# Kernel optimization log

Measured on AMD Instinct MI355X. Metric: run time of the kernel, lower is better.

## Reference

```python
import jax, jax.numpy as jnp
import numpy as np

D = 64      # in_feats
OUT = 64    # out_feats
MEM = 4     # mem_size
NREL = 8    # num_rels
N = 20000   # num nodes
E = 50000   # num edges
FF = 16     # dim_feedforward (hardcoded in module)
NH = 4      # nhead (hardcoded)
EPS = 1e-5  # LayerNorm eps (torch default)


def _ln(x, w, b):
    m = x.mean(-1, keepdims=True)
    v = ((x - m) ** 2).mean(-1, keepdims=True)
    return (x - m) * jax.lax.rsqrt(v + EPS) * w + b


def _enc(x, Wqkv, bqkv, Wo, bo, W1, b1, W2, b2, ln1w, ln1b, ln2w, ln2b):
    # torch TransformerEncoderLayer, batch_first, post-norm, eval mode, no padding mask (all-zero mask)
    B, S, d = x.shape
    dh = d // NH
    qkv = x @ Wqkv.T + bqkv
    q, k, v = jnp.split(qkv, 3, axis=-1)
    q = q.reshape(B, S, NH, dh)
    k = k.reshape(B, S, NH, dh)
    v = v.reshape(B, S, NH, dh)
    att = jax.nn.softmax(jnp.einsum('bqhd,bkhd->bhqk', q, k) / jnp.sqrt(jnp.float32(dh)), axis=-1)
    o = jnp.einsum('bhqk,bkhd->bqhd', att, v).reshape(B, S, d) @ Wo.T + bo
    x = _ln(x + o, ln1w, ln1b)
    ff = jax.nn.relu(x @ W1.T + b1) @ W2.T + b2
    return _ln(x + ff, ln2w, ln2b)


def setup_inputs() -> dict:
    key = jax.random.key(0)
    ks = jax.random.split(key, 16)
    s = 0.05
    inp = {
        'feat': jax.random.normal(ks[0], (N, D), jnp.float32),
        'src_idx': jax.random.randint(ks[1], (E,), 0, N),
        'dst_idx': jax.random.randint(ks[2], (E,), 0, N),
        'etype': jax.random.randint(ks[3], (E,), 0, NREL),
        'Wqkv': jax.random.normal(ks[4], (3 * D, D), jnp.float32) * s,
        'bqkv': jnp.zeros((3 * D,), jnp.float32),
        'Wo': jax.random.normal(ks[5], (D, D), jnp.float32) * s,
        'bo': jnp.zeros((D,), jnp.float32),
        'W1': jax.random.normal(ks[6], (FF, D), jnp.float32) * s,
        'b1': jnp.zeros((FF,), jnp.float32),
        'W2': jax.random.normal(ks[7], (D, FF), jnp.float32) * s,
        'b2': jnp.zeros((D,), jnp.float32),
        'ln1w': jnp.ones((D,), jnp.float32),
        'ln1b': jnp.zeros((D,), jnp.float32),
        'ln2w': jnp.ones((D,), jnp.float32),
        'ln2b': jnp.zeros((D,), jnp.float32),
        'Wc': jax.random.normal(ks[8], (MEM, D), jnp.float32) * s,
        'bc': jnp.zeros((MEM,), jnp.float32),
        'CLS': jax.random.normal(ks[9], (MEM, D), jnp.float32),
        'SEP': jax.random.normal(ks[10], (D,), jnp.float32),
        'Wm': jax.random.normal(ks[11], (OUT * D, D), jnp.float32) * s,
        'h_bias': jnp.zeros((OUT,), jnp.float32),
    }
    return inp


def reference(feat, src_idx, dst_idx, etype, Wqkv, bqkv, Wo, bo, W1, b1, W2, b2,
              ln1w, ln1b, ln2w, ln2b, Wc, bc, CLS, SEP, Wm, h_bias):
    enc_args = (Wqkv, bqkv, Wo, bo, W1, b1, W2, b2, ln1w, ln1b, ln2w, ln2b)

    def cls_pass(s_, d_):
        # run the shared encoder MEM times with a different CLS token; the math
        # is identical for every relation type, so no per-etype partition needed
        B = s_.shape[0]
        outs = []
        mem = jnp.zeros((B, D), s_.dtype)
        for i in range(MEM):
            cls = jnp.broadcast_to(CLS[i], (B, D))[:, None, :]
            sep = jnp.broadcast_to(SEP, (B, D))[:, None, :]
            seq = jnp.concatenate([cls, s_[:, None, :], sep, d_[:, None, :]], axis=1)  # [B,4,D]
            t = _enc(seq, *enc_args)[:, 0, :]
            outs.append(t)
            mem = mem + t
        return mem, jnp.stack(outs)  # [B,D], [MEM,B,D]

    src = feat[src_idx]  # [E,D]
    dst = feat[dst_idx]
    mem_emb, tmps = cls_pass(src, dst)
    cat_all = tmps @ Wc.T + bc               # [MEM,E,MEM]
    w = (mem_emb @ Wm.T).reshape(E, OUT, D)  # per-edge hypernetwork weight
    msg = jnp.einsum('eoi,ei->eo', w, src)   # [E,OUT]

    # dgl fn.mean aggregation over destination nodes (0 for isolated nodes)
    cnt = jax.ops.segment_sum(jnp.ones((E,), msg.dtype), dst_idx, num_segments=N)
    agg = jax.ops.segment_sum(msg, dst_idx, num_segments=N)
    node_rep = jnp.where(cnt[:, None] > 0, agg / jnp.maximum(cnt, 1.0)[:, None], 0.0)
    node_rep = node_rep + h_bias

    # self loop (same hypernetwork path over every node)
    mem_s, _ = cls_pass(feat, feat)
    hs = (mem_s @ Wm.T).reshape(N, OUT, D)
    node_rep = node_rep + jnp.einsum('noi,ni->no', hs, feat)

    # reconstruct torch concat order of category/label: outer loop etype, inner loop mem idx
    et = etype.astype(jnp.int32)
    counts = jax.ops.segment_sum(jnp.ones((E,), jnp.int32), etype, num_segments=NREL)
    start = jnp.concatenate([jnp.zeros((1,), jnp.int32), jnp.cumsum(counts)[:-1].astype(jnp.int32)])
    order = jnp.argsort(etype, stable=True)
    rank = jnp.zeros((E,), jnp.int32).at[order].set(jnp.arange(E, dtype=jnp.int32) - start[et[order]])
    base = start[et] * MEM + rank                                            # [E]
    pos = base[None, :] + jnp.arange(MEM, dtype=jnp.int32)[:, None] * counts[et][None, :]  # [MEM,E]
    category = jnp.zeros((MEM * E, MEM), cat_all.dtype).at[pos.reshape(-1)].set(cat_all.reshape(-1, MEM))
    label = jnp.zeros((MEM * E,), jnp.int32).at[pos.reshape(-1)].set(
        jnp.repeat(jnp.arange(MEM, dtype=jnp.int32), E))
    return node_rep, label, category
```

## Files before the change

### kernel.cpp

```cpp
#include <hip/hip_runtime.h>
#include <hip/hip_bf16.h>

typedef float f32x4_t __attribute__((ext_vector_type(4)));
typedef short bf16x8_t __attribute__((ext_vector_type(8)));

#define MFMA(a, b, c) __builtin_amdgcn_mfma_f32_16x16x32_bf16(a, b, c, 0, 0, 0)

#define C_Q0   0
#define C_S00  256
#define C_S02  272
#define C_VCLS 288
#define C_VSEP 544

__device__ __forceinline__ short f2bf(float x) {
    return (short)__builtin_bit_cast(unsigned short, __float2bfloat16(x));
}
__device__ __forceinline__ float bf2f(short s) {
    return __builtin_bit_cast(float, ((unsigned)(unsigned short)s) << 16);
}
__device__ __forceinline__ float head_sum16(float v) {
#pragma unroll
    for (int off = 1; off < 16; off <<= 1) v += __shfl_xor(v, off, 64);
    return v;
}

__global__ void k_pack(const float* __restrict__ Wo, const float* __restrict__ Wqkv,
                       const float* __restrict__ W1, const float* __restrict__ W2,
                       const float* __restrict__ Wm, const float* __restrict__ Wc,
                       short* __restrict__ Bpack, short* __restrict__ WoP,
                       short* __restrict__ WkvP, short* __restrict__ W1P,
                       short* __restrict__ W2P, short* __restrict__ WcP)
{
    int tid = blockIdx.x * 256 + threadIdx.x;
    short tmp[8];
    if (tid < 32768) {
        int u = tid, lane = u & 63, nt = (u >> 6) & 3, kstep = u >> 8;
        int o = nt * 16 + (lane & 15);
        int kb = kstep * 32 + (lane >> 4) * 8;
#pragma unroll
        for (int t = 0; t < 8; t++) { int k = kb + t; tmp[t] = f2bf(Wm[(o * 64 + (k >> 6)) * 64 + (k & 63)]); }
        *(bf16x8_t*)&Bpack[(size_t)u * 8] = *(bf16x8_t*)tmp;
    } else if (tid < 33280) {
        int u = tid - 32768, lane = u & 63, nt = (u >> 6) & 3, kstep = u >> 8;
        int o = nt * 16 + (lane & 15), kb = kstep * 32 + (lane >> 4) * 8;
#pragma unroll
        for (int t = 0; t < 8; t++) tmp[t] = f2bf(Wo[o * 64 + kb + t]);
        *(bf16x8_t*)&WoP[(size_t)u * 8] = *(bf16x8_t*)tmp;
    } else if (tid < 34304) {
        int u = tid - 33280, lane = u & 63, nt = (u >> 6) & 7, kstep = u >> 9;
        int col = nt * 16 + (lane & 15), kb = kstep * 32 + (lane >> 4) * 8;
        int row = 64 + col;
#pragma unroll
        for (int t = 0; t < 8; t++) tmp[t] = f2bf(Wqkv[row * 64 + kb + t]);
        *(bf16x8_t*)&WkvP[(size_t)u * 8] = *(bf16x8_t*)tmp;
    } else if (tid < 34432) {
        int u = tid - 34304, lane = u & 63, kstep = u >> 6;
        int f = lane & 15, kb = kstep * 32 + (lane >> 4) * 8;
#pragma unroll
        for (int t = 0; t < 8; t++) tmp[t] = f2bf(W1[f * 64 + kb + t]);
        *(bf16x8_t*)&W1P[(size_t)u * 8] = *(bf16x8_t*)tmp;
    } else if (tid < 34688) {
        int u = tid - 34432, lane = u & 63, nt = u >> 6;
        int o = nt * 16 + (lane & 15), kb = (lane >> 4) * 8;
#pragma unroll
        for (int t = 0; t < 8; t++) { int k = kb + t; tmp[t] = (k < 16) ? f2bf(W2[o * 16 + k]) : (short)0; }
        *(bf16x8_t*)&W2P[(size_t)u * 8] = *(bf16x8_t*)tmp;
    } else if (tid < 34816) {
        int u = tid - 34688, lane = u & 63, kstep = u >> 6;
        int m = lane & 15, kb = kstep * 32 + (lane >> 4) * 8;
#pragma unroll
        for (int t = 0; t < 8; t++) tmp[t] = (m < 4) ? f2bf(Wc[m * 64 + kb + t]) : (short)0;
        *(bf16x8_t*)&WcP[(size_t)u * 8] = *(bf16x8_t*)tmp;
    }
}

__global__ void k_small(const float* __restrict__ Wqkv, const float* __restrict__ bqkv,
                        const float* __restrict__ CLS, const float* __restrict__ SEP,
                        float* __restrict__ consts)
{
    int lane = threadIdx.x;
    float ksep = bqkv[64 + lane], vsep = bqkv[128 + lane];
    for (int c = 0; c < 64; c++) {
        float sc = SEP[c];
        ksep += Wqkv[(64 + lane) * 64 + c] * sc;
        vsep += Wqkv[(128 + lane) * 64 + c] * sc;
    }
    consts[C_VSEP + lane] = vsep;
    for (int i = 0; i < 4; i++) {
        float q0 = bqkv[lane], kcls = bqkv[64 + lane], vcls = bqkv[128 + lane];
        for (int c = 0; c < 64; c++) {
            float cc = CLS[i * 64 + c];
            q0   += Wqkv[lane * 64 + c] * cc;
            kcls += Wqkv[(64 + lane) * 64 + c] * cc;
            vcls += Wqkv[(128 + lane) * 64 + c] * cc;
        }
        consts[C_Q0 + i * 64 + lane] = q0;
        consts[C_VCLS + i * 64 + lane] = vcls;
        float p00 = head_sum16(q0 * kcls) * 0.25f;
        float p02 = head_sum16(q0 * ksep) * 0.25f;
        if ((lane & 15) == 0) {
            consts[C_S00 + i * 4 + (lane >> 4)] = p00;
            consts[C_S02 + i * 4 + (lane >> 4)] = p02;
        }
    }
}

__global__ __launch_bounds__(256) void k_kv(const float* __restrict__ feat,
        const short* __restrict__ WkvP, const float* __restrict__ bqkv,
        float* __restrict__ knode, float* __restrict__ vnode, int N)
{
    __shared__ __align__(16) short sA[64 * 72];
    int tid = threadIdx.x, lane = tid & 63, w = tid >> 6;
    int l15 = lane & 15, lh = lane >> 4;
    int base = blockIdx.x * 64;
#pragma unroll
    for (int rr = 0; rr < 16; rr++) {
        int row = w * 16 + rr;
        int n = base + row; n = n < N ? n : N - 1;
        sA[row * 72 + lane] = f2bf(feat[(size_t)n * 64 + lane]);
    }
    __syncthreads();
    const bf16x8_t* bp = (const bf16x8_t*)WkvP;
    bf16x8_t bk0 = bp[(0 * 8 + w) * 64 + lane];
    bf16x8_t bk1 = bp[(1 * 8 + w) * 64 + lane];
    bf16x8_t bv0 = bp[(0 * 8 + 4 + w) * 64 + lane];
    bf16x8_t bv1 = bp[(1 * 8 + 4 + w) * 64 + lane];
    int kof = lh * 8;
    int col = w * 16 + l15;
    float biask = bqkv[64 + col], biasv = bqkv[128 + col];
#pragma unroll
    for (int rt = 0; rt < 4; rt++) {
        bf16x8_t a0 = *(const bf16x8_t*)&sA[(rt * 16 + l15) * 72 + kof];
        bf16x8_t a1 = *(const bf16x8_t*)&sA[(rt * 16 + l15) * 72 + 32 + kof];
        f32x4_t ak = {0.f, 0.f, 0.f, 0.f}, av = ak;
        ak = MFMA(a0, bk0, ak); ak = MFMA(a1, bk1, ak);
        av = MFMA(a0, bv0, av); av = MFMA(a1, bv1, av);
#pragma unroll
        for (int r = 0; r < 4; r++) {
            int n = base + rt * 16 + lh * 4 + r;
            if (n < N) {
                knode[(size_t)n * 64 + col] = ak[r] + biask;
                vnode[(size_t)n * 64 + col] = av[r] + biasv;
            }
        }
    }
}

struct EncW {
    const float* consts; const float* CLS; const float* bo;
    const float* b1; const float* b2;
    const float* ln1w; const float* ln1b; const float* ln2w; const float* ln2b;
    const short* WoP; const short* W1P; const short* W2P; const short* WcP;
    const float* bc;
};

__global__ __launch_bounds__(256) void k_enc(const int* __restrict__ src_idx,
        const int* __restrict__ dst_idx,
        const float* __restrict__ knode, const float* __restrict__ vnode, EncW W,
        float* __restrict__ mem_out, float* __restrict__ cat_out, int E, int M)
{
    __shared__ __align__(16) short sA[64 * 72];
    __shared__ __align__(16) short sF[64 * 40];
    int tid = threadIdx.x, lane = tid & 63, w = tid >> 6;
    int l15 = lane & 15, lh = lane >> 4;
    int base = blockIdx.x * 16;

#pragma unroll
    for (int z = 0; z < 4; z++) {
        int zz = z * 64 + lane;
        sF[(w * 16 + (zz >> 4)) * 40 + 16 + (zz & 15)] = 0;
    }

    float q0r[4], vclsr[4], s00r[4], s02r[4];
#pragma unroll
    for (int i = 0; i < 4; i++) {
        q0r[i]   = W.consts[C_Q0 + i * 64 + lane];
        vclsr[i] = W.consts[C_VCLS + i * 64 + lane];
        s00r[i]  = W.consts[C_S00 + i * 4 + lh];
        s02r[i]  = W.consts[C_S02 + i * 4 + lh];
    }
    float vsep = W.consts[C_VSEP + lane];

#pragma unroll
    for (int el = 0; el < 4; el++) {
        int eloc = w * 4 + el;
        int ge = base + eloc; int gc = ge < M ? ge : M - 1;
        int s, d;
        if (gc < E) { s = src_idx[gc]; d = dst_idx[gc]; }
        else        { s = gc - E; d = s; }
        float ks = knode[(size_t)s * 64 + lane], vs_ = vnode[(size_t)s * 64 + lane];
        float kd = knode[(size_t)d * 64 + lane], vd  = vnode[(size_t)d * 64 + lane];
#pragma unroll
        for (int i = 0; i < 4; i++) {
            float s01 = head_sum16(q0r[i] * ks) * 0.25f;
            float s03 = head_sum16(q0r[i] * kd) * 0.25f;
            float s00 = s00r[i], s02 = s02r[i];
            float mx = fmaxf(fmaxf(s00, s01), fmaxf(s02, s03));
            float e0 = __expf(s00 - mx), e1 = __expf(s01 - mx);
            float e2 = __expf(s02 - mx), e3 = __expf(s03 - mx);
            float inv = 1.0f / (e0 + e1 + e2 + e3);
            float att = (e0 * vclsr[i] + e1 * vs_ + e2 * vsep + e3 * vd) * inv;
            sA[(eloc * 4 + i) * 72 + lane] = f2bf(att);
        }
    }

    int arow = (w * 16 + l15) * 72;
    int kof = lh * 8;

    const bf16x8_t* bpo = (const bf16x8_t*)W.WoP;
    f32x4_t ac0 = {0.f,0.f,0.f,0.f}, ac1 = ac0, ac2 = ac0, ac3 = ac0;
#pragma unroll
    for (int kstep = 0; kstep < 2; kstep++) {
        bf16x8_t a = *(const bf16x8_t*)&sA[arow + kstep * 32 + kof];
        ac0 = MFMA(a, bpo[(kstep * 4 + 0) * 64 + lane], ac0);
        ac1 = MFMA(a, bpo[(kstep * 4 + 1) * 64 + lane], ac1);
        ac2 = MFMA(a, bpo[(kstep * 4 + 2) * 64 + lane], ac2);
        ac3 = MFMA(a, bpo[(kstep * 4 + 3) * 64 + lane], ac3);
    }

    float x[4][4], y[4][4];
#pragma unroll
    for (int r = 0; r < 4; r++) { x[0][r] = ac0[r]; x[1][r] = ac1[r]; x[2][r] = ac2[r]; x[3][r] = ac3[r]; }
    float lw1[4], lb1[4];
#pragma unroll
    for (int nt = 0; nt < 4; nt++) {
        float b = W.bo[nt * 16 + l15];
        lw1[nt] = W.ln1w[nt * 16 + l15]; lb1[nt] = W.ln1b[nt * 16 + l15];
#pragma unroll
        for (int r = 0; r < 4; r++) x[nt][r] += b + W.CLS[r * 64 + nt * 16 + l15];
    }
#pragma unroll
    for (int r = 0; r < 4; r++) {
        float sm = head_sum16(x[0][r] + x[1][r] + x[2][r] + x[3][r]);
        float mu = sm * 0.015625f;
        float vv = 0.f;
#pragma unroll
        for (int nt = 0; nt < 4; nt++) { float dd = x[nt][r] - mu; vv = fmaf(dd, dd, vv); }
        vv = head_sum16(vv);
        float rs = rsqrtf(vv * 0.015625f + 1e-5f);
#pragma unroll
        for (int nt = 0; nt < 4; nt++) y[nt][r] = (x[nt][r] - mu) * rs * lw1[nt] + lb1[nt];
    }
#pragma unroll
    for (int nt = 0; nt < 4; nt++)
#pragma unroll
        for (int r = 0; r < 4; r++)
            sA[(w * 16 + lh * 4 + r) * 72 + nt * 16 + l15] = f2bf(y[nt][r]);

    const bf16x8_t* bp1 = (const bf16x8_t*)W.W1P;
    f32x4_t fa = {0.f,0.f,0.f,0.f};
#pragma unroll
    for (int kstep = 0; kstep < 2; kstep++) {
        bf16x8_t a = *(const bf16x8_t*)&sA[arow + kstep * 32 + kof];
        fa = MFMA(a, bp1[kstep * 64 + lane], fa);
    }
    float b1v = W.b1[l15];
#pragma unroll
    for (int r = 0; r < 4; r++)
        sF[(w * 16 + lh * 4 + r) * 40 + l15] = f2bf(fmaxf(fa[r] + b1v, 0.f));

    const bf16x8_t* bp2 = (const bf16x8_t*)W.W2P;
    bf16x8_t af = *(const bf16x8_t*)&sF[(w * 16 + l15) * 40 + kof];
    f32x4_t z0 = {0.f,0.f,0.f,0.f}, z1 = z0, z2 = z0, z3 = z0;
    z0 = MFMA(af, bp2[0 * 64 + lane], z0);
    z1 = MFMA(af, bp2[1 * 64 + lane], z1);
    z2 = MFMA(af, bp2[2 * 64 + lane], z2);
    z3 = MFMA(af, bp2[3 * 64 + lane], z3);

    float t[4][4];
#pragma unroll
    for (int r = 0; r < 4; r++) { x[0][r] = z0[r]; x[1][r] = z1[r]; x[2][r] = z2[r]; x[3][r] = z3[r]; }
    float lw2[4], lb2[4];
#pragma unroll
    for (int nt = 0; nt < 4; nt++) {
        float b = W.b2[nt * 16 + l15];
        lw2[nt] = W.ln2w[nt * 16 + l15]; lb2[nt] = W.ln2b[nt * 16 + l15];
#pragma unroll
        for (int r = 0; r < 4; r++) x[nt][r] += b + y[nt][r];
    }
#pragma unroll
    for (int r = 0; r < 4; r++) {
        float sm = head_sum16(x[0][r] + x[1][r] + x[2][r] + x[3][r]);
        float mu = sm * 0.015625f;
        float vv = 0.f;
#pragma unroll
        for (int nt = 0; nt < 4; nt++) { float dd = x[nt][r] - mu; vv = fmaf(dd, dd, vv); }
        vv = head_sum16(vv);
        float rs = rsqrtf(vv * 0.015625f + 1e-5f);
#pragma unroll
        for (int nt = 0; nt < 4; nt++) t[nt][r] = (x[nt][r] - mu) * rs * lw2[nt] + lb2[nt];
    }

    int eloc = w * 4 + lh, ge = base + eloc;

    if (base < E) {
#pragma unroll
        for (int nt = 0; nt < 4; nt++)
#pragma unroll
            for (int r = 0; r < 4; r++)
                sA[(w * 16 + lh * 4 + r) * 72 + nt * 16 + l15] = f2bf(t[nt][r]);
        const bf16x8_t* bpc = (const bf16x8_t*)W.WcP;
        f32x4_t ca = {0.f,0.f,0.f,0.f};
#pragma unroll
        for (int kstep = 0; kstep < 2; kstep++) {
            bf16x8_t a = *(const bf16x8_t*)&sA[arow + kstep * 32 + kof];
            ca = MFMA(a, bpc[kstep * 64 + lane], ca);
        }
        if (l15 < 4 && ge < E) {
            float bcv = W.bc[l15];
#pragma unroll
            for (int r = 0; r < 4; r++)
                cat_out[((size_t)r * E + ge) * 4 + l15] = ca[r] + bcv;
        }
    }

    if (ge < M) {
#pragma unroll
        for (int nt = 0; nt < 4; nt++)
            mem_out[(size_t)ge * 64 + nt * 16 + l15] = t[nt][0] + t[nt][1] + t[nt][2] + t[nt][3];
    }
}

__global__ __launch_bounds__(256, 3) void k_hyper(
        const float* __restrict__ feat, const int* __restrict__ src_idx,
        const int* __restrict__ dst_idx, const float* __restrict__ memall,
        const short* __restrict__ Bpack,
        float* __restrict__ agg, float* __restrict__ selfm, int E, int M)
{
    __shared__ short xsT[64 * 132];
    __shared__ __align__(16) short sB[2][8192];
    int tid = threadIdx.x, lane = tid & 63, w = tid >> 6;
    int l15 = lane & 15, lh = lane >> 4, koff = lh * 8;
    int base = blockIdx.x * 128;

    const bf16x8_t* bp = (const bf16x8_t*)Bpack;

    auto stage = [&](int c, int buf) {
#pragma unroll
        for (int jj = 0; jj < 4; ++jj) {
            int j = w * 4 + jj;
            int il_ic = j >> 3, q = j & 7;
            const short* src = (const short*)(bp + (size_t)(c * 2 + il_ic) * 512
                                              + (q >> 2) * 256 + (q & 3) * 64 + lane);
            short* dst = &sB[buf][j * 512];
            __builtin_amdgcn_global_load_lds(
                (const __attribute__((address_space(1))) void*)src,
                (__attribute__((address_space(3))) void*)dst, 16, 0, 0);
        }
    };

    stage(0, 0);

    for (int rr = 0; rr < 32; ++rr) {
        int row = w * 32 + rr, gr = base + row;
        float xv = 0.f;
        if (gr < M) {
            int xi = gr < E ? src_idx[gr] : gr - E;
            xv = feat[(size_t)xi * 64 + lane];
        }
        xsT[lane * 132 + row] = f2bf(xv);
    }

    bf16x8_t am[2][2];
#pragma unroll
    for (int tt = 0; tt < 2; ++tt) {
        int gr = base + w * 32 + tt * 16 + l15;
        const float* mp = memall + (size_t)(gr < M ? gr : 0) * 64 + koff;
#pragma unroll
        for (int kk = 0; kk < 2; ++kk)
#pragma unroll
            for (int t = 0; t < 8; ++t)
                am[tt][kk][t] = f2bf(mp[kk * 32 + t]);
    }

    f32x4_t out[2][4];
#pragma unroll
    for (int tt = 0; tt < 2; ++tt)
#pragma unroll
        for (int nt = 0; nt < 4; ++nt) out[tt][nt] = (f32x4_t){0.f, 0.f, 0.f, 0.f};
    const f32x4_t ZERO = {0.f, 0.f, 0.f, 0.f};

    int xrow0 = w * 32 + lh * 4;

    int cur = 0;
    for (int c = 0; c < 32; ++c) {
        if (c + 1 < 32) {
            stage(c + 1, cur ^ 1);
            asm volatile("s_waitcnt vmcnt(4)" ::: "memory");
        } else {
            asm volatile("s_waitcnt vmcnt(0)" ::: "memory");
        }
        __builtin_amdgcn_s_barrier();
#pragma unroll
        for (int ic = 0; ic < 2; ++ic) {
            int i = c * 2 + ic;
            unsigned long long xw0 = *(const unsigned long long*)&xsT[i * 132 + xrow0];
            unsigned long long xw1 = *(const unsigned long long*)&xsT[i * 132 + xrow0 + 16];
            float x0[4], x1[4];
            {
                unsigned lo0 = (unsigned)xw0, hi0 = (unsigned)(xw0 >> 32);
                unsigned lo1 = (unsigned)xw1, hi1 = (unsigned)(xw1 >> 32);
                x0[0] = __builtin_bit_cast(float, lo0 << 16);
                x0[1] = __builtin_bit_cast(float, lo0 & 0xffff0000u);
                x0[2] = __builtin_bit_cast(float, hi0 << 16);
                x0[3] = __builtin_bit_cast(float, hi0 & 0xffff0000u);
                x1[0] = __builtin_bit_cast(float, lo1 << 16);
                x1[1] = __builtin_bit_cast(float, lo1 & 0xffff0000u);
                x1[2] = __builtin_bit_cast(float, hi1 << 16);
                x1[3] = __builtin_bit_cast(float, hi1 & 0xffff0000u);
            }
            const bf16x8_t* bfr = (const bf16x8_t*)&sB[cur][ic * 4096];
            f32x4_t P0[4], P1[4];
            __builtin_amdgcn_s_setprio(1);
#pragma unroll
            for (int nt = 0; nt < 4; ++nt) {
                bf16x8_t B0 = bfr[nt * 64 + lane];
                bf16x8_t B1 = bfr[(4 + nt) * 64 + lane];
                P0[nt] = MFMA(am[0][0], B0, ZERO);
                P1[nt] = MFMA(am[1][0], B0, ZERO);
                P0[nt] = MFMA(am[0][1], B1, P0[nt]);
                P1[nt] = MFMA(am[1][1], B1, P1[nt]);
            }
            __builtin_amdgcn_s_setprio(0);
#pragma unroll
            for (int nt = 0; nt < 4; ++nt)
#pragma unroll
                for (int r = 0; r < 4; ++r) {
                    out[0][nt][r] = fmaf(x0[r], P0[nt][r], out[0][nt][r]);
                    out[1][nt][r] = fmaf(x1[r], P1[nt][r], out[1][nt][r]);
                }
        }
        __builtin_amdgcn_s_barrier();
        cur ^= 1;
    }

#pragma unroll
    for (int tt = 0; tt < 2; ++tt) {
        int orow = w * 32 + tt * 16 + lh * 4;
        int di[4];
#pragma unroll
        for (int r = 0; r < 4; ++r) {
            int grow = base + orow + r;
            di[r] = (grow < E) ? dst_idx[grow] : 0;
        }
#pragma unroll
        for (int nt = 0; nt < 4; ++nt) {
            int o = nt * 16 + l15;
#pragma unroll
            for (int r = 0; r < 4; ++r) {
                int grow = base + orow + r;
                if (grow < M) {
                    float v = out[tt][nt][r];
                    if (grow < E) atomicAdd(&agg[(size_t)di[r] * 64 + o], v);
                    else selfm[(size_t)(grow - E) * 64 + o] = v;
                }
            }
        }
    }
}

__global__ void k_fin(const float* __restrict__ agg, const int* __restrict__ cnt,
                      const float* __restrict__ selfm, const float* __restrict__ h_bias,
                      float* __restrict__ outp, int N)
{
    int t = blockIdx.x * 256 + threadIdx.x;
    if (t < N * 64) {
        int n = t >> 6, o = t & 63;
        int c = cnt[n];
        float av = (c > 0) ? agg[t] / (float)c : 0.f;
        outp[t] = av + h_bias[o] + selfm[t];
    }
}

__global__ void k_hist(const int* __restrict__ etype, const int* __restrict__ dst,
                       int* __restrict__ hist, int* __restrict__ cnt, int E)
{
    __shared__ int h[8];
    int tid = threadIdx.x;
    if (tid < 8) h[tid] = 0;
    __syncthreads();
    int e = blockIdx.x * 256 + tid;
    if (e < E) {
        atomicAdd(&h[etype[e]], 1);
        atomicAdd(&cnt[dst[e]], 1);
    }
    __syncthreads();
    if (tid < 8) hist[blockIdx.x * 8 + tid] = h[tid];
}

__global__ void k_scan(const int* __restrict__ hist, int* __restrict__ chunkoff,
                       int* __restrict__ startg, int* __restrict__ countsg, int nch)
{
    int lane = threadIdx.x;
    int g = lane & 7, seg = lane >> 3;
    int per = (nch + 7) / 8;
    int c0 = seg * per, c1 = c0 + per; if (c1 > nch) c1 = nch;
    int sum = 0;
    for (int c = c0; c < c1; c++) sum += hist[c * 8 + g];
    int pre = 0, tot = 0;
#pragma unroll
    for (int s2 = 0; s2 < 8; s2++) {
        int v = __shfl(sum, s2 * 8 + g, 64);
        tot += v;
        if (s2 < seg) pre += v;
    }
    int run = pre;
    for (int c = c0; c < c1; c++) { chunkoff[c * 8 + g] = run; run += hist[c * 8 + g]; }
    if (seg == 0) {
        countsg[g] = tot;
        int sg = 0;
#pragma unroll
        for (int g2 = 0; g2 < 8; g2++) { int v = __shfl(tot, g2, 64); if (g2 < g) sg += v; }
        startg[g] = sg;
    }
}

__global__ __launch_bounds__(256) void k_scatter(const int* __restrict__ etype,
        const float* __restrict__ cat_all,
        const int* __restrict__ chunkoff, const int* __restrict__ startg,
        const int* __restrict__ countsg,
        float* __restrict__ out_label, float* __restrict__ out_cat, int E)
{
    __shared__ int wc[4][8];
    int tid = threadIdx.x, lane = tid & 63, w = tid >> 6;
    int chunk = blockIdx.x;
    int e = chunk * 256 + w * 64 + lane;
    int et = (e < E) ? etype[e] : -1;
    unsigned long long mk[8];
#pragma unroll
    for (int g = 0; g < 8; g++) mk[g] = __ballot(et == g);
    if (lane < 8) wc[w][lane] = (int)__popcll(mk[lane]);
    __syncthreads();
    if (et >= 0) {
        unsigned long long lt = (1ull << lane) - 1ull;
        int myr = chunkoff[chunk * 8 + et] + (int)__popcll(mk[et] & lt);
#pragma unroll
        for (int w2 = 0; w2 < 4; w2++) if (w2 < w) myr += wc[w2][et];
        int sg = startg[et], cg = countsg[et];
        size_t pbase = (size_t)sg * 4 + myr;
#pragma unroll
        for (int i = 0; i < 4; i++) {
            size_t pos = pbase + (size_t)i * cg;
            out_label[pos] = (float)i;
            const float* ca = &cat_all[((size_t)i * E + e) * 4];
            float4 cv = {ca[0], ca[1], ca[2], ca[3]};
            *(float4*)&out_cat[pos * 4] = cv;
        }
    }
}

extern "C" void kernel_launch(void* const* d_in, const int* in_sizes, int n_in,
                              void* d_out, int out_size, void* d_ws, size_t ws_size,
                              hipStream_t stream)
{
    const float* feat    = (const float*)d_in[0];
    const int*   src_idx = (const int*)d_in[1];
    const int*   dst_idx = (const int*)d_in[2];
    const int*   etype   = (const int*)d_in[3];
    const float* Wqkv    = (const float*)d_in[4];
    const float* bqkv    = (const float*)d_in[5];
    const float* Wo      = (const float*)d_in[6];
    const float* bo      = (const float*)d_in[7];
    const float* W1      = (const float*)d_in[8];
    const float* b1      = (const float*)d_in[9];
    const float* W2      = (const float*)d_in[10];
    const float* b2      = (const float*)d_in[11];
    const float* ln1w    = (const float*)d_in[12];
    const float* ln1b    = (const float*)d_in[13];
    const float* ln2w    = (const float*)d_in[14];
    const float* ln2b    = (const float*)d_in[15];
    const float* Wc      = (const float*)d_in[16];
    const float* bc      = (const float*)d_in[17];
    const float* CLS     = (const float*)d_in[18];
    const float* SEP     = (const float*)d_in[19];
    const float* Wm      = (const float*)d_in[20];
    const float* h_bias  = (const float*)d_in[21];

    const int N = in_sizes[0] / 64;
    const int E = in_sizes[1];
    const int M = E + N;
    const int NCH = (E + 255) / 256;

    float* ws = (float*)d_ws;
    size_t off = 0;
    auto alloc = [&](size_t n) { float* p = ws + off; off += (n + 63) & ~(size_t)63; return p; };
    float* knode   = alloc((size_t)N * 64);
    float* vnode   = alloc((size_t)N * 64);
    float* mem_all = alloc((size_t)M * 64);
    float* cat_all = alloc((size_t)E * 16);
    float* agg     = alloc((size_t)N * 64 + N);
    int*   cnt     = (int*)(agg + (size_t)N * 64);
    float* selfm   = alloc((size_t)N * 64);
    float* consts  = alloc(1024);
    short* Bpack   = (short*)alloc(131072);
    short* WoP     = (short*)alloc(2048);
    short* WkvP    = (short*)alloc(4096);
    short* W1P     = (short*)alloc(512);
    short* W2P     = (short*)alloc(1024);
    short* WcP     = (short*)alloc(512);
    int*   hist    = (int*)alloc(NCH * 8);
    int*   chunkoff= (int*)alloc(NCH * 8);
    int*   startg  = (int*)alloc(8);
    int*   countsg = (int*)alloc(8);

    float* out_node  = (float*)d_out;
    float* out_label = out_node + (size_t)N * 64;
    float* out_cat   = out_label + (size_t)4 * E;

    hipMemsetAsync(agg, 0, ((size_t)N * 64 + N) * sizeof(float), stream);

    k_pack<<<136, 256, 0, stream>>>(Wo, Wqkv, W1, W2, Wm, Wc, Bpack, WoP, WkvP, W1P, W2P, WcP);
    k_small<<<1, 64, 0, stream>>>(Wqkv, bqkv, CLS, SEP, consts);
    k_hist<<<NCH, 256, 0, stream>>>(etype, dst_idx, hist, cnt, E);
    k_scan<<<1, 64, 0, stream>>>(hist, chunkoff, startg, countsg, NCH);

    k_kv<<<(N + 63) / 64, 256, 0, stream>>>(feat, WkvP, bqkv, knode, vnode, N);

    EncW W{consts, CLS, bo, b1, b2, ln1w, ln1b, ln2w, ln2b, WoP, W1P, W2P, WcP, bc};

    k_enc<<<(M + 15) / 16, 256, 0, stream>>>(src_idx, dst_idx, knode, vnode, W,
                                             mem_all, cat_all, E, M);

    k_hyper<<<(M + 127) / 128, 256, 0, stream>>>(feat, src_idx, dst_idx, mem_all, Bpack,
                                                 agg, selfm, E, M);

    k_fin<<<(N * 64 + 255) / 256, 256, 0, stream>>>(agg, cnt, selfm, h_bias, out_node, N);

    k_scatter<<<NCH, 256, 0, stream>>>(etype, cat_all, chunkoff, startg, countsg,
                                       out_label, out_cat, E);
}
```

Baseline: 165.3 us.

## Merge prep kernels and widen hypernetwork tile to 256 rows with 512 threads

Three small setup kernels (weight packing, constant computation, histogram) are fused into one launch by dispatching on block index, which removes launch gaps. The hypernetwork kernel now processes 256 rows per block with 8 waves, so each staged Bpack chunk is reused across twice as many rows and global weight traffic is halved. The staging granularity drops to one i-slice per iteration, using a single barrier per step with a full vmcnt wait. Shorter prefetch chunks and more barriers per row could expose load latency, and the larger block may reduce occupancy.

```diff
diff --git a/kernel.cpp b/kernel.cpp
--- a/kernel.cpp
+++ b/kernel.cpp
@@ -24,84 +24,102 @@
     return v;
 }
 
-__global__ void k_pack(const float* __restrict__ Wo, const float* __restrict__ Wqkv,
+__global__ void k_prep(const float* __restrict__ Wo, const float* __restrict__ Wqkv,
                        const float* __restrict__ W1, const float* __restrict__ W2,
                        const float* __restrict__ Wm, const float* __restrict__ Wc,
+                       const float* __restrict__ bqkv,
+                       const float* __restrict__ CLS, const float* __restrict__ SEP,
+                       const int* __restrict__ etype, const int* __restrict__ dst,
                        short* __restrict__ Bpack, short* __restrict__ WoP,
                        short* __restrict__ WkvP, short* __restrict__ W1P,
-                       short* __restrict__ W2P, short* __restrict__ WcP)
-{
-    int tid = blockIdx.x * 256 + threadIdx.x;
-    short tmp[8];
-    if (tid < 32768) {
-        int u = tid, lane = u & 63, nt = (u >> 6) & 3, kstep = u >> 8;
-        int o = nt * 16 + (lane & 15);
-        int kb = kstep * 32 + (lane >> 4) * 8;
-#pragma unroll
-        for (int t = 0; t < 8; t++) { int k = kb + t; tmp[t] = f2bf(Wm[(o * 64 + (k >> 6)) * 64 + (k & 63)]); }
-        *(bf16x8_t*)&Bpack[(size_t)u * 8] = *(bf16x8_t*)tmp;
-    } else if (tid < 33280) {
-        int u = tid - 32768, lane = u & 63, nt = (u >> 6) & 3, kstep = u >> 8;
-        int o = nt * 16 + (lane & 15), kb = kstep * 32 + (lane >> 4) * 8;
-#pragma unroll
-        for (int t = 0; t < 8; t++) tmp[t] = f2bf(Wo[o * 64 + kb + t]);
-        *(bf16x8_t*)&WoP[(size_t)u * 8] = *(bf16x8_t*)tmp;
-    } else if (tid < 34304) {
-        int u = tid - 33280, lane = u & 63, nt = (u >> 6) & 7, kstep = u >> 9;
-        int col = nt * 16 + (lane & 15), kb = kstep * 32 + (lane >> 4) * 8;
-        int row = 64 + col;
-#pragma unroll
-        for (int t = 0; t < 8; t++) tmp[t] = f2bf(Wqkv[row * 64 + kb + t]);
-        *(bf16x8_t*)&WkvP[(size_t)u * 8] = *(bf16x8_t*)tmp;
-    } else if (tid < 34432) {
-        int u = tid - 34304, lane = u & 63, kstep = u >> 6;
-        int f = lane & 15, kb = kstep * 32 + (lane >> 4) * 8;
-#pragma unroll
-        for (int t = 0; t < 8; t++) tmp[t] = f2bf(W1[f * 64 + kb + t]);
-        *(bf16x8_t*)&W1P[(size_t)u * 8] = *(bf16x8_t*)tmp;
-    } else if (tid < 34688) {
-        int u = tid - 34432, lane = u & 63, nt = u >> 6;
-        int o = nt * 16 + (lane & 15), kb = (lane >> 4) * 8;
-#pragma unroll
-        for (int t = 0; t < 8; t++) { int k = kb + t; tmp[t] = (k < 16) ? f2bf(W2[o * 16 + k]) : (short)0; }
-        *(bf16x8_t*)&W2P[(size_t)u * 8] = *(bf16x8_t*)tmp;
-    } else if (tid < 34816) {
-        int u = tid - 34688, lane = u & 63, kstep = u >> 6;
-        int m = lane & 15, kb = kstep * 32 + (lane >> 4) * 8;
-#pragma unroll
-        for (int t = 0; t < 8; t++) tmp[t] = (m < 4) ? f2bf(Wc[m * 64 + kb + t]) : (short)0;
-        *(bf16x8_t*)&WcP[(size_t)u * 8] = *(bf16x8_t*)tmp;
-    }
-}
-
-__global__ void k_small(const float* __restrict__ Wqkv, const float* __restrict__ bqkv,
-                        const float* __restrict__ CLS, const float* __restrict__ SEP,
-                        float* __restrict__ consts)
-{
-    int lane = threadIdx.x;
-    float ksep = bqkv[64 + lane], vsep = bqkv[128 + lane];
-    for (int c = 0; c < 64; c++) {
-        float sc = SEP[c];
-        ksep += Wqkv[(64 + lane) * 64 + c] * sc;
-        vsep += Wqkv[(128 + lane) * 64 + c] * sc;
-    }
-    consts[C_VSEP + lane] = vsep;
-    for (int i = 0; i < 4; i++) {
-        float q0 = bqkv[lane], kcls = bqkv[64 + lane], vcls = bqkv[128 + lane];
-        for (int c = 0; c < 64; c++) {
-            float cc = CLS[i * 64 + c];
-            q0   += Wqkv[lane * 64 + c] * cc;
-            kcls += Wqkv[(64 + lane) * 64 + c] * cc;
-            vcls += Wqkv[(128 + lane) * 64 + c] * cc;
-        }
-        consts[C_Q0 + i * 64 + lane] = q0;
-        consts[C_VCLS + i * 64 + lane] = vcls;
-        float p00 = head_sum16(q0 * kcls) * 0.25f;
-        float p02 = head_sum16(q0 * ksep) * 0.25f;
-        if ((lane & 15) == 0) {
-            consts[C_S00 + i * 4 + (lane >> 4)] = p00;
-            consts[C_S02 + i * 4 + (lane >> 4)] = p02;
-        }
+                       short* __restrict__ W2P, short* __restrict__ WcP,
+                       float* __restrict__ consts,
+                       int* __restrict__ hist, int* __restrict__ cnt, int E)
+{
+    int bx = blockIdx.x;
+    if (bx < 136) {
+        int tid = bx * 256 + threadIdx.x;
+        short tmp[8];
+        if (tid < 32768) {
+            int u = tid, lane = u & 63, nt = (u >> 6) & 3, kstep = u >> 8;
+            int o = nt * 16 + (lane & 15);
+            int kb = kstep * 32 + (lane >> 4) * 8;
+#pragma unroll
+            for (int t = 0; t < 8; t++) { int k = kb + t; tmp[t] = f2bf(Wm[(o * 64 + (k >> 6)) * 64 + (k & 63)]); }
+            *(bf16x8_t*)&Bpack[(size_t)u * 8] = *(bf16x8_t*)tmp;
+        } else if (tid < 33280) {
+            int u = tid - 32768, lane = u & 63, nt = (u >> 6) & 3, kstep = u >> 8;
+            int o = nt * 16 + (lane & 15), kb = kstep * 32 + (lane >> 4) * 8;
+#pragma unroll
+            for (int t = 0; t < 8; t++) tmp[t] = f2bf(Wo[o * 64 + kb + t]);
+            *(bf16x8_t*)&WoP[(size_t)u * 8] = *(bf16x8_t*)tmp;
+        } else if (tid < 34304) {
+            int u = tid - 33280, lane = u & 63, nt = (u >> 6) & 7, kstep = u >> 9;
+            int col = nt * 16 + (lane & 15), kb = kstep * 32 + (lane >> 4) * 8;
+            int row = 64 + col;
+#pragma unroll
+            for (int t = 0; t < 8; t++) tmp[t] = f2bf(Wqkv[row * 64 + kb + t]);
+            *(bf16x8_t*)&WkvP[(size_t)u * 8] = *(bf16x8_t*)tmp;
+        } else if (tid < 34432) {
+            int u = tid - 34304, lane = u & 63, kstep = u >> 6;
+            int f = lane & 15, kb = kstep * 32 + (lane >> 4) * 8;
+#pragma unroll
+            for (int t = 0; t < 8; t++) tmp[t] = f2bf(W1[f * 64 + kb + t]);
+            *(bf16x8_t*)&W1P[(size_t)u * 8] = *(bf16x8_t*)tmp;
+        } else if (tid < 34688) {
+            int u = tid - 34432, lane = u & 63, nt = u >> 6;
+            int o = nt * 16 + (lane & 15), kb = (lane >> 4) * 8;
+#pragma unroll
+            for (int t = 0; t < 8; t++) { int k = kb + t; tmp[t] = (k < 16) ? f2bf(W2[o * 16 + k]) : (short)0; }
+            *(bf16x8_t*)&W2P[(size_t)u * 8] = *(bf16x8_t*)tmp;
+        } else if (tid < 34816) {
+            int u = tid - 34688, lane = u & 63, kstep = u >> 6;
+            int m = lane & 15, kb = kstep * 32 + (lane >> 4) * 8;
+#pragma unroll
+            for (int t = 0; t < 8; t++) tmp[t] = (m < 4) ? f2bf(Wc[m * 64 + kb + t]) : (short)0;
+            *(bf16x8_t*)&WcP[(size_t)u * 8] = *(bf16x8_t*)tmp;
+        }
+    } else if (bx == 136) {
+        if (threadIdx.x < 64) {
+            int lane = threadIdx.x;
+            float ksep = bqkv[64 + lane], vsep = bqkv[128 + lane];
+            for (int c = 0; c < 64; c++) {
+                float sc = SEP[c];
+                ksep += Wqkv[(64 + lane) * 64 + c] * sc;
+                vsep += Wqkv[(128 + lane) * 64 + c] * sc;
+            }
+            consts[C_VSEP + lane] = vsep;
+            for (int i = 0; i < 4; i++) {
+                float q0 = bqkv[lane], kcls = bqkv[64 + lane], vcls = bqkv[128 + lane];
+                for (int c = 0; c < 64; c++) {
+                    float cc = CLS[i * 64 + c];
+                    q0   += Wqkv[lane * 64 + c] * cc;
+                    kcls += Wqkv[(64 + lane) * 64 + c] * cc;
+                    vcls += Wqkv[(128 + lane) * 64 + c] * cc;
+                }
+                consts[C_Q0 + i * 64 + lane] = q0;
+                consts[C_VCLS + i * 64 + lane] = vcls;
+                float p00 = head_sum16(q0 * kcls) * 0.25f;
+                float p02 = head_sum16(q0 * ksep) * 0.25f;
+                if ((lane & 15) == 0) {
+                    consts[C_S00 + i * 4 + (lane >> 4)] = p00;
+                    consts[C_S02 + i * 4 + (lane >> 4)] = p02;
+                }
+            }
+        }
+    } else {
+        __shared__ int h[8];
+        int chunk = bx - 137;
+        int tid = threadIdx.x;
+        if (tid < 8) h[tid] = 0;
+        __syncthreads();
+        int e = chunk * 256 + tid;
+        if (e < E) {
+            atomicAdd(&h[etype[e]], 1);
+            atomicAdd(&cnt[dst[e]], 1);
+        }
+        __syncthreads();
+        if (tid < 8) hist[chunk * 8 + tid] = h[tid];
     }
 }
 
@@ -321,32 +339,26 @@
     }
 }
 
-__global__ __launch_bounds__(256, 3) void k_hyper(
+__global__ __launch_bounds__(512, 4) void k_hyper(
         const float* __restrict__ feat, const int* __restrict__ src_idx,
         const int* __restrict__ dst_idx, const float* __restrict__ memall,
         const short* __restrict__ Bpack,
         float* __restrict__ agg, float* __restrict__ selfm, int E, int M)
 {
-    __shared__ short xsT[64 * 132];
-    __shared__ __align__(16) short sB[2][8192];
+    __shared__ short xsT[64 * 260];
+    __shared__ __align__(16) short sB[2][4096];
     int tid = threadIdx.x, lane = tid & 63, w = tid >> 6;
     int l15 = lane & 15, lh = lane >> 4, koff = lh * 8;
-    int base = blockIdx.x * 128;
+    int base = blockIdx.x * 256;
 
     const bf16x8_t* bp = (const bf16x8_t*)Bpack;
 
-    auto stage = [&](int c, int buf) {
-#pragma unroll
-        for (int jj = 0; jj < 4; ++jj) {
-            int j = w * 4 + jj;
-            int il_ic = j >> 3, q = j & 7;
-            const short* src = (const short*)(bp + (size_t)(c * 2 + il_ic) * 512
-                                              + (q >> 2) * 256 + (q & 3) * 64 + lane);
-            short* dst = &sB[buf][j * 512];
-            __builtin_amdgcn_global_load_lds(
-                (const __attribute__((address_space(1))) void*)src,
-                (__attribute__((address_space(3))) void*)dst, 16, 0, 0);
-        }
+    auto stage = [&](int i, int buf) {
+        const short* src = (const short*)(bp + (size_t)i * 512 + w * 64 + lane);
+        short* dst = &sB[buf][w * 512];
+        __builtin_amdgcn_global_load_lds(
+            (const __attribute__((address_space(1))) void*)src,
+            (__attribute__((address_space(3))) void*)dst, 16, 0, 0);
     };
 
     stage(0, 0);
@@ -358,7 +370,7 @@
             int xi = gr < E ? src_idx[gr] : gr - E;
             xv = feat[(size_t)xi * 64 + lane];
         }
-        xsT[lane * 132 + row] = f2bf(xv);
+        xsT[lane * 260 + row] = f2bf(xv);
     }
 
     bf16x8_t am[2][2];
@@ -383,54 +395,46 @@
     int xrow0 = w * 32 + lh * 4;
 
     int cur = 0;
-    for (int c = 0; c < 32; ++c) {
-        if (c + 1 < 32) {
-            stage(c + 1, cur ^ 1);
-            asm volatile("s_waitcnt vmcnt(4)" ::: "memory");
-        } else {
-            asm volatile("s_waitcnt vmcnt(0)" ::: "memory");
-        }
+    for (int i = 0; i < 64; ++i) {
+        asm volatile("s_waitcnt vmcnt(0)" ::: "memory");
         __builtin_amdgcn_s_barrier();
-#pragma unroll
-        for (int ic = 0; ic < 2; ++ic) {
-            int i = c * 2 + ic;
-            unsigned long long xw0 = *(const unsigned long long*)&xsT[i * 132 + xrow0];
-            unsigned long long xw1 = *(const unsigned long long*)&xsT[i * 132 + xrow0 + 16];
-            float x0[4], x1[4];
-            {
-                unsigned lo0 = (unsigned)xw0, hi0 = (unsigned)(xw0 >> 32);
-                unsigned lo1 = (unsigned)xw1, hi1 = (unsigned)(xw1 >> 32);
-                x0[0] = __builtin_bit_cast(float, lo0 << 16);
-                x0[1] = __builtin_bit_cast(float, lo0 & 0xffff0000u);
-                x0[2] = __builtin_bit_cast(float, hi0 << 16);
-                x0[3] = __builtin_bit_cast(float, hi0 & 0xffff0000u);
-                x1[0] = __builtin_bit_cast(float, lo1 << 16);
-                x1[1] = __builtin_bit_cast(float, lo1 & 0xffff0000u);
-                x1[2] = __builtin_bit_cast(float, hi1 << 16);
-                x1[3] = __builtin_bit_cast(float, hi1 & 0xffff0000u);
+        if (i + 1 < 64) stage(i + 1, cur ^ 1);
+
+        unsigned long long xw0 = *(const unsigned long long*)&xsT[i * 260 + xrow0];
+        unsigned long long xw1 = *(const unsigned long long*)&xsT[i * 260 + xrow0 + 16];
+        float x0[4], x1[4];
+        {
+            unsigned lo0 = (unsigned)xw0, hi0 = (unsigned)(xw0 >> 32);
+            unsigned lo1 = (unsigned)xw1, hi1 = (unsigned)(xw1 >> 32);
+            x0[0] = __builtin_bit_cast(float, lo0 << 16);
+            x0[1] = __builtin_bit_cast(float, lo0 & 0xffff0000u);
+            x0[2] = __builtin_bit_cast(float, hi0 << 16);
+            x0[3] = __builtin_bit_cast(float, hi0 & 0xffff0000u);
+            x1[0] = __builtin_bit_cast(float, lo1 << 16);
+            x1[1] = __builtin_bit_cast(float, lo1 & 0xffff0000u);
+            x1[2] = __builtin_bit_cast(float, hi1 << 16);
+            x1[3] = __builtin_bit_cast(float, hi1 & 0xffff0000u);
+        }
+        const bf16x8_t* bfr = (const bf16x8_t*)sB[cur];
+        f32x4_t P0[4], P1[4];
+        __builtin_amdgcn_s_setprio(1);
+#pragma unroll
+        for (int nt = 0; nt < 4; ++nt) {
+            bf16x8_t B0 = bfr[nt * 64 + lane];
+            bf16x8_t B1 = bfr[(4 + nt) * 64 + lane];
+            P0[nt] = MFMA(am[0][0], B0, ZERO);
+            P1[nt] = MFMA(am[1][0], B0, ZERO);
+            P0[nt] = MFMA(am[0][1], B1, P0[nt]);
+            P1[nt] = MFMA(am[1][1], B1, P1[nt]);
+        }
+        __builtin_amdgcn_s_setprio(0);
+#pragma unroll
+        for (int nt = 0; nt < 4; ++nt)
+#pragma unroll
+            for (int r = 0; r < 4; ++r) {
+                out[0][nt][r] = fmaf(x0[r], P0[nt][r], out[0][nt][r]);
+                out[1][nt][r] = fmaf(x1[r], P1[nt][r], out[1][nt][r]);
             }
-            const bf16x8_t* bfr = (const bf16x8_t*)&sB[cur][ic * 4096];
-            f32x4_t P0[4], P1[4];
-            __builtin_amdgcn_s_setprio(1);
-#pragma unroll
-            for (int nt = 0; nt < 4; ++nt) {
-                bf16x8_t B0 = bfr[nt * 64 + lane];
-                bf16x8_t B1 = bfr[(4 + nt) * 64 + lane];
-                P0[nt] = MFMA(am[0][0], B0, ZERO);
-                P1[nt] = MFMA(am[1][0], B0, ZERO);
-                P0[nt] = MFMA(am[0][1], B1, P0[nt]);
-                P1[nt] = MFMA(am[1][1], B1, P1[nt]);
-            }
-            __builtin_amdgcn_s_setprio(0);
-#pragma unroll
-            for (int nt = 0; nt < 4; ++nt)
-#pragma unroll
-                for (int r = 0; r < 4; ++r) {
-                    out[0][nt][r] = fmaf(x0[r], P0[nt][r], out[0][nt][r]);
-                    out[1][nt][r] = fmaf(x1[r], P1[nt][r], out[1][nt][r]);
-                }
-        }
-        __builtin_amdgcn_s_barrier();
         cur ^= 1;
     }
 
@@ -470,22 +474,6 @@
         float av = (c > 0) ? agg[t] / (float)c : 0.f;
         outp[t] = av + h_bias[o] + selfm[t];
     }
-}
-
-__global__ void k_hist(const int* __restrict__ etype, const int* __restrict__ dst,
-                       int* __restrict__ hist, int* __restrict__ cnt, int E)
-{
-    __shared__ int h[8];
-    int tid = threadIdx.x;
-    if (tid < 8) h[tid] = 0;
-    __syncthreads();
-    int e = blockIdx.x * 256 + tid;
-    if (e < E) {
-        atomicAdd(&h[etype[e]], 1);
-        atomicAdd(&cnt[dst[e]], 1);
-    }
-    __syncthreads();
-    if (tid < 8) hist[blockIdx.x * 8 + tid] = h[tid];
 }
 
 __global__ void k_scan(const int* __restrict__ hist, int* __restrict__ chunkoff,
@@ -609,9 +597,9 @@
 
     hipMemsetAsync(agg, 0, ((size_t)N * 64 + N) * sizeof(float), stream);
 
-    k_pack<<<136, 256, 0, stream>>>(Wo, Wqkv, W1, W2, Wm, Wc, Bpack, WoP, WkvP, W1P, W2P, WcP);
-    k_small<<<1, 64, 0, stream>>>(Wqkv, bqkv, CLS, SEP, consts);
-    k_hist<<<NCH, 256, 0, stream>>>(etype, dst_idx, hist, cnt, E);
+    k_prep<<<137 + NCH, 256, 0, stream>>>(Wo, Wqkv, W1, W2, Wm, Wc, bqkv, CLS, SEP,
+                                          etype, dst_idx, Bpack, WoP, WkvP, W1P, W2P, WcP,
+                                          consts, hist, cnt, E);
     k_scan<<<1, 64, 0, stream>>>(hist, chunkoff, startg, countsg, NCH);
 
     k_kv<<<(N + 63) / 64, 256, 0, stream>>>(feat, WkvP, bqkv, knode, vnode, N);
@@ -621,7 +609,7 @@
     k_enc<<<(M + 15) / 16, 256, 0, stream>>>(src_idx, dst_idx, knode, vnode, W,
                                              mem_all, cat_all, E, M);
 
-    k_hyper<<<(M + 127) / 128, 256, 0, stream>>>(feat, src_idx, dst_idx, mem_all, Bpack,
+    k_hyper<<<(M + 255) / 256, 512, 0, stream>>>(feat, src_idx, dst_idx, mem_all, Bpack,
                                                  agg, selfm, E, M);
 
     k_fin<<<(N * 64 + 255) / 256, 256, 0, stream>>>(agg, cnt, selfm, h_bias, out_node, N);
```

Result: slower. 171.8 us (+3.9%).
